# Optimization experiments

Measured on AMD Instinct MI355X. Metric: run time of the kernel, lower is better.

Reference implementation:

```python
import jax, jax.numpy as jnp
import numpy as np

N_NODES = 50000
N_EDGES = 800000
IN_DIM = 128
HID = 64
OUT_DIM = 128
N_GRAPHS = 256


def setup_inputs() -> dict:
    key = jax.random.key(0)
    ks = jax.random.split(key, 8)
    x = jax.random.normal(ks[0], (N_NODES, IN_DIM), dtype=jnp.float32)
    edge_index = jax.random.randint(ks[1], (2, N_EDGES), 0, N_NODES, dtype=jnp.int64)
    batch = jnp.sort(jax.random.randint(ks[2], (N_NODES,), 0, N_GRAPHS, dtype=jnp.int64))
    # Glorot-ish init for GCN weights, zero bias (PyG default bias=True)
    W1 = jax.random.normal(ks[3], (IN_DIM, HID), dtype=jnp.float32) / np.sqrt(IN_DIM)
    b1 = jnp.zeros((HID,), dtype=jnp.float32)
    W2 = jax.random.normal(ks[4], (HID, HID), dtype=jnp.float32) / np.sqrt(HID)
    b2 = jnp.zeros((HID,), dtype=jnp.float32)
    W3 = jax.random.normal(ks[5], (HID, OUT_DIM), dtype=jnp.float32) / np.sqrt(HID)
    b3 = jnp.zeros((OUT_DIM,), dtype=jnp.float32)
    return {"x": x, "edge_index": edge_index, "batch": batch, "num_graphs": N_GRAPHS,
            "W1": W1, "b1": b1, "W2": W2, "b2": b2, "W3": W3, "b3": b3}


def _gcn_norm(edge_index, n_nodes):
    # PyG GCNConv default: add self-loops, symmetric D^{-1/2}(A+I)D^{-1/2} norm.
    loops = jnp.arange(n_nodes, dtype=edge_index.dtype)
    src = jnp.concatenate([edge_index[0], loops])  # [E + N]
    dst = jnp.concatenate([edge_index[1], loops])
    deg = jax.ops.segment_sum(jnp.ones_like(dst, dtype=jnp.float32), dst,
                              num_segments=n_nodes)
    dinv = jnp.where(deg > 0, jax.lax.rsqrt(jnp.maximum(deg, 1.0)), 0.0)
    norm = dinv[src] * dinv[dst]  # [E + N]
    return src, dst, norm


def _gcn_conv(x, W, b, src, dst, norm, n_nodes):
    h = x @ W                                  # [N, F_out] dense GEMM
    msg = h[src] * norm[:, None]               # gather + scale  [E+N, F_out]
    agg = jax.ops.segment_sum(msg, dst, num_segments=n_nodes)
    return agg + b


def reference(x, edge_index, batch, num_graphs, W1, b1, W2, b2, W3, b3):
    n_nodes = x.shape[0]
    src, dst, norm = _gcn_norm(edge_index, n_nodes)
    h = jax.nn.gelu(_gcn_conv(x, W1, b1, src, dst, norm, n_nodes))
    h = jax.nn.gelu(_gcn_conv(h, W2, b2, src, dst, norm, n_nodes))
    h = _gcn_conv(h, W3, b3, src, dst, norm, n_nodes)
    # global_mean_pool over batch segment ids
    sums = jax.ops.segment_sum(h, batch, num_segments=num_graphs)
    counts = jax.ops.segment_sum(jnp.ones((n_nodes,), dtype=h.dtype), batch,
                                 num_segments=num_graphs)
    return sums / jnp.maximum(counts, 1.0)[:, None]
```

## Files before the change

kernel.cpp:

```cpp
#include <hip/hip_runtime.h>
#include <hip/hip_fp16.h>
#include <math.h>

#define N_NODES   50000
#define N_EDGES   800000
#define IN_DIM    128
#define HID       64
#define OUT_DIM   128
#define N_GRAPHS  256
#define MAX_DEG   64
#define PARTS     8
#define PSIZE     (N_NODES / PARTS)
#define EPB       4096
#define AGG_NPB   32
#define GEMM_BLKS 782

typedef _Float16 half8 __attribute__((ext_vector_type(8)));
typedef float floatx4 __attribute__((ext_vector_type(4)));


__global__ __launch_bounds__(256) void k_prep_w(const float* __restrict__ W1, __half* __restrict__ Wt1,
                                                const float* __restrict__ W2, __half* __restrict__ Wt2) {
    int blk = blockIdx.x;
    if (blk < 4) {
        int idx = blk * 256 + threadIdx.x;
        int g = idx >> 6, n = idx & 63;
#pragma unroll
        for (int i = 0; i < 8; i++)
            Wt1[idx * 8 + i] = __float2half(W1[(8 * g + i) * 64 + n]);
    } else {
        int idx = (blk - 4) * 256 + threadIdx.x;
        if (idx < 512) {
            int g = idx >> 6, n = idx & 63;
#pragma unroll
            for (int i = 0; i < 8; i++)
                Wt2[idx * 8 + i] = __float2half(W2[(8 * g + i) * 64 + n]);
        }
    }
}


__global__ __launch_bounds__(256) void k_fused1(const float* __restrict__ A,
                                                const __half* __restrict__ Bp,
                                                __half* __restrict__ C,
                                                const int* __restrict__ src,
                                                const int* __restrict__ dst,
                                                int* __restrict__ deg,
                                                int* __restrict__ col) {
    if (blockIdx.x < GEMM_BLKS) {
        constexpr int K = IN_DIM, S = K / 32;
        int wv   = threadIdx.x >> 6;
        int lane = threadIdx.x & 63;
        int quad = lane >> 4, l15 = lane & 15;
        int row0 = blockIdx.x * 64 + wv * 16;
        if (row0 >= N_NODES) return;

        half8 bf[S][4];
#pragma unroll
        for (int s = 0; s < S; s++)
#pragma unroll
            for (int j = 0; j < 4; j++)
                bf[s][j] = *(const half8*)(Bp + ((size_t)((4 * s + quad) * 64 + 16 * j + l15)) * 8);

        floatx4 acc[4];
#pragma unroll
        for (int j = 0; j < 4; j++) acc[j] = 0.f;

        int arow = row0 + l15;
#pragma unroll
        for (int s = 0; s < S; s++) {
            float4 xa = *(const float4*)(A + (size_t)arow * K + 32 * s + quad * 8);
            float4 xb = *(const float4*)(A + (size_t)arow * K + 32 * s + quad * 8 + 4);
            half8 af;
            af[0] = (_Float16)xa.x; af[1] = (_Float16)xa.y;
            af[2] = (_Float16)xa.z; af[3] = (_Float16)xa.w;
            af[4] = (_Float16)xb.x; af[5] = (_Float16)xb.y;
            af[6] = (_Float16)xb.z; af[7] = (_Float16)xb.w;
#pragma unroll
            for (int j = 0; j < 4; j++)
                acc[j] = __builtin_amdgcn_mfma_f32_16x16x32_f16(af, bf[s][j], acc[j], 0, 0, 0);
        }
#pragma unroll
        for (int j = 0; j < 4; j++)
#pragma unroll
            for (int r = 0; r < 4; r++)
                C[(size_t)(row0 + quad * 4 + r) * 64 + 16 * j + l15] = __float2half(acc[j][r]);
    } else {
        int bid   = blockIdx.x - GEMM_BLKS;
        int p     = bid & (PARTS - 1);
        int chunk = bid >> 3;
        int e0    = chunk * EPB + threadIdx.x * 16;
        if (e0 + 16 > N_EDGES) return;
        int lo = p * PSIZE, hi = lo + PSIZE;

        int dd[16], ss[16];
        const int4* d4 = (const int4*)(dst + e0);
        const int4* s4 = (const int4*)(src + e0);
#pragma unroll
        for (int j = 0; j < 4; j++) {
            int4 q = d4[j];
            dd[4 * j + 0] = q.x; dd[4 * j + 1] = q.y;
            dd[4 * j + 2] = q.z; dd[4 * j + 3] = q.w;
        }
#pragma unroll
        for (int j = 0; j < 4; j++) {
            int4 q = s4[j];
            ss[4 * j + 0] = q.x; ss[4 * j + 1] = q.y;
            ss[4 * j + 2] = q.z; ss[4 * j + 3] = q.w;
        }

        int pos[16];
#pragma unroll
        for (int j = 0; j < 16; j++) {
            pos[j] = -1;
            if (dd[j] >= lo && dd[j] < hi) pos[j] = atomicAdd(&deg[dd[j]], 1);
        }
#pragma unroll
        for (int j = 0; j < 16; j++) {
            if (pos[j] >= 0 && pos[j] < MAX_DEG)
                col[(size_t)dd[j] * MAX_DEG + pos[j]] = ss[j];
        }
    }
}


__global__ __launch_bounds__(256) void k_prep2(const int* __restrict__ deg,
                                               float* __restrict__ dinv) {
    int n = blockIdx.x * 256 + threadIdx.x;
    if (n < N_NODES) dinv[n] = rsqrtf((float)(deg[n] + 1));
}


__global__ __launch_bounds__(256) void k_mfma2(const __half* __restrict__ A,
                                               const __half* __restrict__ Bp,
                                               __half* __restrict__ C) {
    constexpr int K = HID, S = K / 32;
    int wv   = threadIdx.x >> 6;
    int lane = threadIdx.x & 63;
    int quad = lane >> 4, l15 = lane & 15;
    int row0 = blockIdx.x * 64 + wv * 16;
    if (row0 >= N_NODES) return;

    half8 bf[S][4];
#pragma unroll
    for (int s = 0; s < S; s++)
#pragma unroll
        for (int j = 0; j < 4; j++)
            bf[s][j] = *(const half8*)(Bp + ((size_t)((4 * s + quad) * 64 + 16 * j + l15)) * 8);

    floatx4 acc[4];
#pragma unroll
    for (int j = 0; j < 4; j++) acc[j] = 0.f;

    int arow = row0 + l15;
#pragma unroll
    for (int s = 0; s < S; s++) {
        half8 af = *(const half8*)(A + (size_t)arow * K + 32 * s + quad * 8);
#pragma unroll
        for (int j = 0; j < 4; j++)
            acc[j] = __builtin_amdgcn_mfma_f32_16x16x32_f16(af, bf[s][j], acc[j], 0, 0, 0);
    }
#pragma unroll
    for (int j = 0; j < 4; j++)
#pragma unroll
        for (int r = 0; r < 4; r++)
            C[(size_t)(row0 + quad * 4 + r) * 64 + 16 * j + l15] = __float2half(acc[j][r]);
}


__device__ __forceinline__ void fma8(float* acc, uint4 v, float w) {
    const __half2* h = (const __half2*)&v;
#pragma unroll
    for (int j = 0; j < 4; j++) {
        acc[2 * j]     += w * __low2float(h[j]);
        acc[2 * j + 1] += w * __high2float(h[j]);
    }
}

__global__ __launch_bounds__(256) void k_agg(const __half* __restrict__ T,
                                             const int* __restrict__ col,
                                             const int* __restrict__ indeg,
                                             const float* __restrict__ dinv,
                                             const float* __restrict__ b,
                                             __half* __restrict__ OUT,
                                             int mode, int scale_src) {
    __shared__ int cols[AGG_NPB][MAX_DEG + 1];
    __shared__ int sdeg[AGG_NPB];
    int base = blockIdx.x * AGG_NPB;

    if (threadIdx.x < AGG_NPB) {
        int g = base + threadIdx.x;
        int dg0 = (g < N_NODES) ? indeg[g] : 0;
        sdeg[threadIdx.x] = dg0 > MAX_DEG ? MAX_DEG : dg0;
    }
    __syncthreads();

    for (int idx = threadIdx.x; idx < AGG_NPB * MAX_DEG; idx += 256) {
        int r = idx >> 6, j = idx & 63;
        if (j < sdeg[r]) cols[r][j] = col[(size_t)(base + r) * MAX_DEG + j];
    }
    __syncthreads();

    int lane = threadIdx.x & 63;
    int wv   = threadIdx.x >> 6;
    int q = lane >> 3, t = lane & 7;
    int local = wv * 8 + q;
    int d = base + local;
    if (d >= N_NODES) return;

    int dg = sdeg[local];
    float dv = dinv[d];

    float acc[8];
#pragma unroll
    for (int j = 0; j < 8; j++) acc[j] = 0.f;
    fma8(acc, *(const uint4*)(T + (size_t)d * HID + t * 8), scale_src ? dv : 1.0f);

    const int* cl = cols[local];
    int i = 0;
    for (; i + 4 <= dg; i += 4) {
        int s0 = cl[i], s1 = cl[i + 1], s2 = cl[i + 2], s3 = cl[i + 3];
        uint4 v0 = *(const uint4*)(T + (size_t)s0 * HID + t * 8);
        uint4 v1 = *(const uint4*)(T + (size_t)s1 * HID + t * 8);
        uint4 v2 = *(const uint4*)(T + (size_t)s2 * HID + t * 8);
        uint4 v3 = *(const uint4*)(T + (size_t)s3 * HID + t * 8);
        float w0 = 1.f, w1 = 1.f, w2 = 1.f, w3 = 1.f;
        if (scale_src) { w0 = dinv[s0]; w1 = dinv[s1]; w2 = dinv[s2]; w3 = dinv[s3]; }
        fma8(acc, v0, w0); fma8(acc, v1, w1); fma8(acc, v2, w2); fma8(acc, v3, w3);
    }
    for (; i < dg; i++) {
        int s = cl[i];
        float w = scale_src ? dinv[s] : 1.f;
        fma8(acc, *(const uint4*)(T + (size_t)s * HID + t * 8), w);
    }

    float o[8];
#pragma unroll
    for (int j = 0; j < 8; j++) o[j] = acc[j] * dv;
    if (mode == 0) {
#pragma unroll
        for (int j = 0; j < 8; j++) {
            float v = o[j] + b[t * 8 + j];
            float u2 = 0.7978845608028654f * (v + 0.044715f * v * v * v);
            float th = 1.0f - 2.0f / (__expf(2.0f * u2) + 1.0f);
            o[j] = 0.5f * v * (1.0f + th) * dv;
        }
    }
    __half2 hh[4];
#pragma unroll
    for (int j = 0; j < 4; j++) hh[j] = __floats2half2_rn(o[2 * j], o[2 * j + 1]);
    *(uint4*)(OUT + (size_t)d * HID + t * 8) = *(uint4*)hh;
}


__global__ __launch_bounds__(256) void k_pool_out(const __half* __restrict__ A,
                                                  const int* __restrict__ batch,
                                                  const float* __restrict__ W3,
                                                  const float* __restrict__ b3,
                                                  float* __restrict__ out) {
    int g = blockIdx.x;
    int lo = 0, hi = N_NODES;
    while (lo < hi) { int m = (lo + hi) >> 1; if (batch[m] < g) lo = m + 1; else hi = m; }
    int lo2 = lo, hi2 = N_NODES;
    while (lo2 < hi2) { int m = (lo2 + hi2) >> 1; if (batch[m] < g + 1) lo2 = m + 1; else hi2 = m; }
    int start = lo, end = lo2;

    int lane = threadIdx.x & 63;
    int wave = threadIdx.x >> 6;
    float acc = 0.f;
    for (int n = start + wave; n < end; n += 4)
        acc += __half2float(A[(size_t)n * HID + lane]);

    __shared__ float part[4][HID];
    __shared__ float pooled[HID];
    part[wave][lane] = acc;
    __syncthreads();
    if (threadIdx.x < HID)
        pooled[threadIdx.x] = part[0][threadIdx.x] + part[1][threadIdx.x] +
                              part[2][threadIdx.x] + part[3][threadIdx.x];
    __syncthreads();

    if (threadIdx.x < OUT_DIM) {
        float cntf = (float)(end - start);
        float inv = 1.0f / fmaxf(cntf, 1.0f);
        float s = 0.f;
#pragma unroll
        for (int k = 0; k < HID; k++) s += pooled[k] * W3[k * OUT_DIM + threadIdx.x];
        out[g * OUT_DIM + threadIdx.x] = (s + cntf * b3[threadIdx.x]) * inv;
    }
}


extern "C" void kernel_launch(void* const* d_in, const int* in_sizes, int n_in,
                              void* d_out, int out_size, void* d_ws, size_t ws_size,
                              hipStream_t stream) {
    const float* x     = (const float*)d_in[0];
    const int*   ei    = (const int*)d_in[1];
    const int*   batch = (const int*)d_in[2];
    const float* W1    = (const float*)d_in[4];
    const float* b1    = (const float*)d_in[5];
    const float* W2    = (const float*)d_in[6];
    const float* b2    = (const float*)d_in[7];
    const float* W3    = (const float*)d_in[8];
    const float* b3    = (const float*)d_in[9];
    float* out = (float*)d_out;

    const int* esrc = ei;
    const int* edst = ei + N_EDGES;

    int*    deg  = (int*)d_ws;
    float*  dinv = (float*)(deg + N_NODES);
    int*    col  = (int*)(dinv + N_NODES);
    __half* t    = (__half*)(col + (size_t)N_NODES * MAX_DEG);
    __half* p    = t + (size_t)N_NODES * HID;
    __half* Wt1  = p + (size_t)N_NODES * HID;
    __half* Wt2  = Wt1 + IN_DIM * HID;

    (void)hipMemsetAsync(deg, 0, (size_t)N_NODES * 4, stream);

    const int CHUNKS = (N_EDGES + EPB - 1) / EPB;
    const int AB = (N_NODES + AGG_NPB - 1) / AGG_NPB;

    k_prep_w<<<6, 256, 0, stream>>>(W1, Wt1, W2, Wt2);
    k_fused1<<<GEMM_BLKS + CHUNKS * PARTS, 256, 0, stream>>>(x, Wt1, t, esrc, edst, deg, col);
    k_prep2<<<196, 256, 0, stream>>>(deg, dinv);

    k_agg<<<AB, 256, 0, stream>>>(t, col, deg, dinv, b1, p, 0, 1);
    k_mfma2<<<GEMM_BLKS, 256, 0, stream>>>(p, Wt2, t);
    k_agg<<<AB, 256, 0, stream>>>(t, col, deg, dinv, b2, p, 0, 0);
    k_agg<<<AB, 256, 0, stream>>>(p, col, deg, dinv, b3, t, 1, 0);
    k_pool_out<<<N_GRAPHS, 256, 0, stream>>>(t, batch, W3, b3, out);
}
```

Measured before the change: 219.8 us.

## Fuse layer-1 aggregation with layer-2 GEMM and compute dinv inline

Folds the layer-2 MFMA GEMM into the first aggregation kernel: each block stages its aggregated, GELU'd rows in shared memory and multiplies them by W2 before writing. It also drops the dinv precompute kernel and array, recomputing rsqrt(deg+1) on the fly from the degree array. This removes two launches and one round trip of the N x 64 intermediate through global memory. In exchange there is an extra gather of indeg per neighbour in the first layer, plus rsqrt arithmetic.

Result: no change. 222.7 us (+1.3%).

```diff
diff --git a/kernel.cpp b/kernel.cpp
--- a/kernel.cpp
+++ b/kernel.cpp
@@ -124,50 +124,6 @@
 }
 
 
-__global__ __launch_bounds__(256) void k_prep2(const int* __restrict__ deg,
-                                               float* __restrict__ dinv) {
-    int n = blockIdx.x * 256 + threadIdx.x;
-    if (n < N_NODES) dinv[n] = rsqrtf((float)(deg[n] + 1));
-}
-
-
-__global__ __launch_bounds__(256) void k_mfma2(const __half* __restrict__ A,
-                                               const __half* __restrict__ Bp,
-                                               __half* __restrict__ C) {
-    constexpr int K = HID, S = K / 32;
-    int wv   = threadIdx.x >> 6;
-    int lane = threadIdx.x & 63;
-    int quad = lane >> 4, l15 = lane & 15;
-    int row0 = blockIdx.x * 64 + wv * 16;
-    if (row0 >= N_NODES) return;
-
-    half8 bf[S][4];
-#pragma unroll
-    for (int s = 0; s < S; s++)
-#pragma unroll
-        for (int j = 0; j < 4; j++)
-            bf[s][j] = *(const half8*)(Bp + ((size_t)((4 * s + quad) * 64 + 16 * j + l15)) * 8);
-
-    floatx4 acc[4];
-#pragma unroll
-    for (int j = 0; j < 4; j++) acc[j] = 0.f;
-
-    int arow = row0 + l15;
-#pragma unroll
-    for (int s = 0; s < S; s++) {
-        half8 af = *(const half8*)(A + (size_t)arow * K + 32 * s + quad * 8);
-#pragma unroll
-        for (int j = 0; j < 4; j++)
-            acc[j] = __builtin_amdgcn_mfma_f32_16x16x32_f16(af, bf[s][j], acc[j], 0, 0, 0);
-    }
-#pragma unroll
-    for (int j = 0; j < 4; j++)
-#pragma unroll
-        for (int r = 0; r < 4; r++)
-            C[(size_t)(row0 + quad * 4 + r) * 64 + 16 * j + l15] = __float2half(acc[j][r]);
-}
-
-
 __device__ __forceinline__ void fma8(float* acc, uint4 v, float w) {
     const __half2* h = (const __half2*)&v;
 #pragma unroll
@@ -177,13 +133,113 @@
     }
 }
 
+
+__global__ __launch_bounds__(256) void k_agg_mm(const __half* __restrict__ T,
+                                                const int* __restrict__ col,
+                                                const int* __restrict__ indeg,
+                                                const float* __restrict__ b,
+                                                const __half* __restrict__ Bp,
+                                                __half* __restrict__ OUT) {
+    __shared__ int cols[AGG_NPB][MAX_DEG + 1];
+    __shared__ int sdeg[AGG_NPB];
+    __shared__ __half p_tile[AGG_NPB][72];
+    int base = blockIdx.x * AGG_NPB;
+
+    if (threadIdx.x < AGG_NPB) {
+        int g = base + threadIdx.x;
+        int dg0 = (g < N_NODES) ? indeg[g] : 0;
+        sdeg[threadIdx.x] = dg0 > MAX_DEG ? MAX_DEG : dg0;
+    }
+    __syncthreads();
+
+    for (int idx = threadIdx.x; idx < AGG_NPB * MAX_DEG; idx += 256) {
+        int r = idx >> 6, j = idx & 63;
+        if (j < sdeg[r]) cols[r][j] = col[(size_t)(base + r) * MAX_DEG + j];
+    }
+    __syncthreads();
+
+    int lane = threadIdx.x & 63;
+    int wv   = threadIdx.x >> 6;
+    int q = lane >> 3, t = lane & 7;
+    int local = wv * 8 + q;
+    int d = base + local;
+
+    if (d < N_NODES) {
+        int dg = sdeg[local];
+        float dv = rsqrtf((float)(indeg[d] + 1));
+
+        float acc[8];
+#pragma unroll
+        for (int j = 0; j < 8; j++) acc[j] = 0.f;
+        fma8(acc, *(const uint4*)(T + (size_t)d * HID + t * 8), dv);
+
+        const int* cl = cols[local];
+        int i = 0;
+        for (; i + 4 <= dg; i += 4) {
+            int s0 = cl[i], s1 = cl[i + 1], s2 = cl[i + 2], s3 = cl[i + 3];
+            uint4 v0 = *(const uint4*)(T + (size_t)s0 * HID + t * 8);
+            uint4 v1 = *(const uint4*)(T + (size_t)s1 * HID + t * 8);
+            uint4 v2 = *(const uint4*)(T + (size_t)s2 * HID + t * 8);
+            uint4 v3 = *(const uint4*)(T + (size_t)s3 * HID + t * 8);
+            float w0 = rsqrtf((float)(indeg[s0] + 1));
+            float w1 = rsqrtf((float)(indeg[s1] + 1));
+            float w2 = rsqrtf((float)(indeg[s2] + 1));
+            float w3 = rsqrtf((float)(indeg[s3] + 1));
+            fma8(acc, v0, w0); fma8(acc, v1, w1); fma8(acc, v2, w2); fma8(acc, v3, w3);
+        }
+        for (; i < dg; i++) {
+            int s = cl[i];
+            fma8(acc, *(const uint4*)(T + (size_t)s * HID + t * 8), rsqrtf((float)(indeg[s] + 1)));
+        }
+
+        half8 hrow;
+#pragma unroll
+        for (int j = 0; j < 8; j++) {
+            float v = acc[j] * dv + b[t * 8 + j];
+            float u2 = 0.7978845608028654f * (v + 0.044715f * v * v * v);
+            float th = 1.0f - 2.0f / (__expf(2.0f * u2) + 1.0f);
+            hrow[j] = (_Float16)(0.5f * v * (1.0f + th) * dv);
+        }
+        *(half8*)&p_tile[local][t * 8] = hrow;
+    }
+    __syncthreads();
+
+    int quad = lane >> 4, l15 = lane & 15;
+    int rows16 = (wv >> 1) * 16;
+    int j0 = (wv & 1) * 2;
+    if (base + rows16 < N_NODES) {
+        half8 bfr[2][2];
+#pragma unroll
+        for (int s = 0; s < 2; s++)
+#pragma unroll
+            for (int jj = 0; jj < 2; jj++)
+                bfr[s][jj] = *(const half8*)(Bp + ((size_t)((4 * s + quad) * 64 + 16 * (j0 + jj) + l15)) * 8);
+
+        floatx4 acc2[2];
+        acc2[0] = 0.f; acc2[1] = 0.f;
+#pragma unroll
+        for (int s = 0; s < 2; s++) {
+            half8 a = *(const half8*)&p_tile[rows16 + l15][s * 32 + quad * 8];
+            acc2[0] = __builtin_amdgcn_mfma_f32_16x16x32_f16(a, bfr[s][0], acc2[0], 0, 0, 0);
+            acc2[1] = __builtin_amdgcn_mfma_f32_16x16x32_f16(a, bfr[s][1], acc2[1], 0, 0, 0);
+        }
+#pragma unroll
+        for (int jj = 0; jj < 2; jj++)
+#pragma unroll
+            for (int r = 0; r < 4; r++) {
+                int row = base + rows16 + quad * 4 + r;
+                if (row < N_NODES)
+                    OUT[(size_t)row * 64 + 16 * (j0 + jj) + l15] = __float2half(acc2[jj][r]);
+            }
+    }
+}
+
+
 __global__ __launch_bounds__(256) void k_agg(const __half* __restrict__ T,
                                              const int* __restrict__ col,
                                              const int* __restrict__ indeg,
-                                             const float* __restrict__ dinv,
                                              const float* __restrict__ b,
-                                             __half* __restrict__ OUT,
-                                             int mode, int scale_src) {
+                                             __half* __restrict__ OUT, int mode) {
     __shared__ int cols[AGG_NPB][MAX_DEG + 1];
     __shared__ int sdeg[AGG_NPB];
     int base = blockIdx.x * AGG_NPB;
@@ -209,12 +265,12 @@
     if (d >= N_NODES) return;
 
     int dg = sdeg[local];
-    float dv = dinv[d];
+    float dv = rsqrtf((float)(indeg[d] + 1));
 
     float acc[8];
 #pragma unroll
     for (int j = 0; j < 8; j++) acc[j] = 0.f;
-    fma8(acc, *(const uint4*)(T + (size_t)d * HID + t * 8), scale_src ? dv : 1.0f);
+    fma8(acc, *(const uint4*)(T + (size_t)d * HID + t * 8), 1.0f);
 
     const int* cl = cols[local];
     int i = 0;
@@ -224,14 +280,11 @@
         uint4 v1 = *(const uint4*)(T + (size_t)s1 * HID + t * 8);
         uint4 v2 = *(const uint4*)(T + (size_t)s2 * HID + t * 8);
         uint4 v3 = *(const uint4*)(T + (size_t)s3 * HID + t * 8);
-        float w0 = 1.f, w1 = 1.f, w2 = 1.f, w3 = 1.f;
-        if (scale_src) { w0 = dinv[s0]; w1 = dinv[s1]; w2 = dinv[s2]; w3 = dinv[s3]; }
-        fma8(acc, v0, w0); fma8(acc, v1, w1); fma8(acc, v2, w2); fma8(acc, v3, w3);
+        fma8(acc, v0, 1.f); fma8(acc, v1, 1.f); fma8(acc, v2, 1.f); fma8(acc, v3, 1.f);
     }
     for (; i < dg; i++) {
         int s = cl[i];
-        float w = scale_src ? dinv[s] : 1.f;
-        fma8(acc, *(const uint4*)(T + (size_t)s * HID + t * 8), w);
+        fma8(acc, *(const uint4*)(T + (size_t)s * HID + t * 8), 1.f);
     }
 
     float o[8];
@@ -309,8 +362,7 @@
     const int* edst = ei + N_EDGES;
 
     int*    deg  = (int*)d_ws;
-    float*  dinv = (float*)(deg + N_NODES);
-    int*    col  = (int*)(dinv + N_NODES);
+    int*    col  = deg + N_NODES;
     __half* t    = (__half*)(col + (size_t)N_NODES * MAX_DEG);
     __half* p    = t + (size_t)N_NODES * HID;
     __half* Wt1  = p + (size_t)N_NODES * HID;
@@ -323,11 +375,9 @@
 
     k_prep_w<<<6, 256, 0, stream>>>(W1, Wt1, W2, Wt2);
     k_fused1<<<GEMM_BLKS + CHUNKS * PARTS, 256, 0, stream>>>(x, Wt1, t, esrc, edst, deg, col);
-    k_prep2<<<196, 256, 0, stream>>>(deg, dinv);
-
-    k_agg<<<AB, 256, 0, stream>>>(t, col, deg, dinv, b1, p, 0, 1);
-    k_mfma2<<<GEMM_BLKS, 256, 0, stream>>>(p, Wt2, t);
-    k_agg<<<AB, 256, 0, stream>>>(t, col, deg, dinv, b2, p, 0, 0);
-    k_agg<<<AB, 256, 0, stream>>>(p, col, deg, dinv, b3, t, 1, 0);
-    k_pool_out<<<N_GRAPHS, 256, 0, stream>>>(t, batch, W3, b3, out);
-}
+
+    k_agg_mm<<<AB, 256, 0, stream>>>(t, col, deg, b1, Wt2, p);
+    k_agg<<<AB, 256, 0, stream>>>(p, col, deg, b2, t, 0);
+    k_agg<<<AB, 256, 0, stream>>>(t, col, deg, b3, p, 1);
+    k_pool_out<<<N_GRAPHS, 256, 0, stream>>>(p, batch, W3, b3, out);
+}
```

## Split features into two 32-wide planes and fold weight and dinv prep into kernels

Applied to the files above, without the earlier changes.

Node feature buffers are stored as two 32-column half planes. Each aggregation block now handles one plane, with 4 lanes per node instead of 8, so the gathered working set per pass is halved and may stay in cache. The separate weight-transpose and dinv kernels are removed: GEMM blocks convert the weights to half in LDS, and dinv is recomputed with rsqrt from degrees inside aggregation. The LDS staging of column indices is dropped, so neighbour indices are read straight from global memory and every edge pays an extra degree load for the source scaling.

Result: slower. 232.2 us (+5.7%).

```diff
diff --git a/kernel.cpp b/kernel.cpp
--- a/kernel.cpp
+++ b/kernel.cpp
@@ -12,36 +12,16 @@
 #define PARTS     8
 #define PSIZE     (N_NODES / PARTS)
 #define EPB       4096
-#define AGG_NPB   32
+#define AGG_NPB   64
 #define GEMM_BLKS 782
+#define PSTRIDE   ((size_t)N_NODES * 32)
 
 typedef _Float16 half8 __attribute__((ext_vector_type(8)));
 typedef float floatx4 __attribute__((ext_vector_type(4)));
 
 
-__global__ __launch_bounds__(256) void k_prep_w(const float* __restrict__ W1, __half* __restrict__ Wt1,
-                                                const float* __restrict__ W2, __half* __restrict__ Wt2) {
-    int blk = blockIdx.x;
-    if (blk < 4) {
-        int idx = blk * 256 + threadIdx.x;
-        int g = idx >> 6, n = idx & 63;
-#pragma unroll
-        for (int i = 0; i < 8; i++)
-            Wt1[idx * 8 + i] = __float2half(W1[(8 * g + i) * 64 + n]);
-    } else {
-        int idx = (blk - 4) * 256 + threadIdx.x;
-        if (idx < 512) {
-            int g = idx >> 6, n = idx & 63;
-#pragma unroll
-            for (int i = 0; i < 8; i++)
-                Wt2[idx * 8 + i] = __float2half(W2[(8 * g + i) * 64 + n]);
-        }
-    }
-}
-
-
 __global__ __launch_bounds__(256) void k_fused1(const float* __restrict__ A,
-                                                const __half* __restrict__ Bp,
+                                                const float* __restrict__ W1,
                                                 __half* __restrict__ C,
                                                 const int* __restrict__ src,
                                                 const int* __restrict__ dst,
@@ -49,6 +29,21 @@
                                                 int* __restrict__ col) {
     if (blockIdx.x < GEMM_BLKS) {
         constexpr int K = IN_DIM, S = K / 32;
+        __shared__ __half wlds[IN_DIM * HID];
+
+#pragma unroll
+        for (int u = 0; u < 8; u++) {
+            int o = threadIdx.x * 32 + u * 4;
+            float4 w = *(const float4*)(W1 + o);
+            int k = o >> 6, n = o & 63;
+            int bi = (((k >> 3) * 64) + n) * 8 + (k & 7);
+            wlds[bi]      = __float2half(w.x);
+            wlds[bi + 8]  = __float2half(w.y);
+            wlds[bi + 16] = __float2half(w.z);
+            wlds[bi + 24] = __float2half(w.w);
+        }
+        __syncthreads();
+
         int wv   = threadIdx.x >> 6;
         int lane = threadIdx.x & 63;
         int quad = lane >> 4, l15 = lane & 15;
@@ -60,7 +55,7 @@
         for (int s = 0; s < S; s++)
 #pragma unroll
             for (int j = 0; j < 4; j++)
-                bf[s][j] = *(const half8*)(Bp + ((size_t)((4 * s + quad) * 64 + 16 * j + l15)) * 8);
+                bf[s][j] = *(const half8*)&wlds[(((4 * s + quad) * 64) + 16 * j + l15) * 8];
 
         floatx4 acc[4];
 #pragma unroll
@@ -84,7 +79,8 @@
         for (int j = 0; j < 4; j++)
 #pragma unroll
             for (int r = 0; r < 4; r++)
-                C[(size_t)(row0 + quad * 4 + r) * 64 + 16 * j + l15] = __float2half(acc[j][r]);
+                C[(size_t)(j >> 1) * PSTRIDE + (size_t)(row0 + quad * 4 + r) * 32 +
+                  16 * (j & 1) + l15] = __float2half(acc[j][r]);
     } else {
         int bid   = blockIdx.x - GEMM_BLKS;
         int p     = bid & (PARTS - 1);
@@ -124,17 +120,101 @@
 }
 
 
-__global__ __launch_bounds__(256) void k_prep2(const int* __restrict__ deg,
-                                               float* __restrict__ dinv) {
-    int n = blockIdx.x * 256 + threadIdx.x;
-    if (n < N_NODES) dinv[n] = rsqrtf((float)(deg[n] + 1));
+__device__ __forceinline__ void fma8(float* acc, uint4 v, float w) {
+    const __half2* h = (const __half2*)&v;
+#pragma unroll
+    for (int j = 0; j < 4; j++) {
+        acc[2 * j]     += w * __low2float(h[j]);
+        acc[2 * j + 1] += w * __high2float(h[j]);
+    }
+}
+
+
+__global__ __launch_bounds__(256) void k_agg(const __half* __restrict__ T,
+                                             const int* __restrict__ col,
+                                             const int* __restrict__ indeg,
+                                             const float* __restrict__ b,
+                                             __half* __restrict__ OUT,
+                                             int mode, int scale_src) {
+    int plane = blockIdx.x & 1;
+    int base  = (blockIdx.x >> 1) * AGG_NPB;
+    int lane = threadIdx.x & 63;
+    int wv   = threadIdx.x >> 6;
+    int q = lane >> 2, t = lane & 3;
+    int local = wv * 16 + q;
+    int d = base + local;
+    if (d >= N_NODES) return;
+
+    int dgf = indeg[d];
+    int dg = dgf > MAX_DEG ? MAX_DEG : dgf;
+    float dv = rsqrtf((float)(dgf + 1));
+    const __half* P = T + (size_t)plane * PSTRIDE;
+
+    float acc[8];
+#pragma unroll
+    for (int j = 0; j < 8; j++) acc[j] = 0.f;
+    fma8(acc, *(const uint4*)(P + (size_t)d * 32 + t * 8), scale_src ? dv : 1.0f);
+
+    const int* cl = col + (size_t)d * MAX_DEG;
+    int i = 0;
+    for (; i + 4 <= dg; i += 4) {
+        int s0 = cl[i], s1 = cl[i + 1], s2 = cl[i + 2], s3 = cl[i + 3];
+        uint4 v0 = *(const uint4*)(P + (size_t)s0 * 32 + t * 8);
+        uint4 v1 = *(const uint4*)(P + (size_t)s1 * 32 + t * 8);
+        uint4 v2 = *(const uint4*)(P + (size_t)s2 * 32 + t * 8);
+        uint4 v3 = *(const uint4*)(P + (size_t)s3 * 32 + t * 8);
+        float w0 = 1.f, w1 = 1.f, w2 = 1.f, w3 = 1.f;
+        if (scale_src) {
+            w0 = rsqrtf((float)(indeg[s0] + 1));
+            w1 = rsqrtf((float)(indeg[s1] + 1));
+            w2 = rsqrtf((float)(indeg[s2] + 1));
+            w3 = rsqrtf((float)(indeg[s3] + 1));
+        }
+        fma8(acc, v0, w0); fma8(acc, v1, w1); fma8(acc, v2, w2); fma8(acc, v3, w3);
+    }
+    for (; i < dg; i++) {
+        int s = cl[i];
+        float w = scale_src ? rsqrtf((float)(indeg[s] + 1)) : 1.f;
+        fma8(acc, *(const uint4*)(P + (size_t)s * 32 + t * 8), w);
+    }
+
+    float o[8];
+#pragma unroll
+    for (int j = 0; j < 8; j++) o[j] = acc[j] * dv;
+    if (mode == 0) {
+#pragma unroll
+        for (int j = 0; j < 8; j++) {
+            float v = o[j] + b[plane * 32 + t * 8 + j];
+            float u2 = 0.7978845608028654f * (v + 0.044715f * v * v * v);
+            float th = 1.0f - 2.0f / (__expf(2.0f * u2) + 1.0f);
+            o[j] = 0.5f * v * (1.0f + th) * dv;
+        }
+    }
+    __half2 hh[4];
+#pragma unroll
+    for (int j = 0; j < 4; j++) hh[j] = __floats2half2_rn(o[2 * j], o[2 * j + 1]);
+    *(uint4*)(OUT + (size_t)plane * PSTRIDE + (size_t)d * 32 + t * 8) = *(uint4*)hh;
 }
 
 
 __global__ __launch_bounds__(256) void k_mfma2(const __half* __restrict__ A,
-                                               const __half* __restrict__ Bp,
+                                               const float* __restrict__ W2,
                                                __half* __restrict__ C) {
-    constexpr int K = HID, S = K / 32;
+    constexpr int S = HID / 32;
+    __shared__ __half wlds[HID * HID];
+#pragma unroll
+    for (int u = 0; u < 4; u++) {
+        int o = threadIdx.x * 16 + u * 4;
+        float4 w = *(const float4*)(W2 + o);
+        int k = o >> 6, n = o & 63;
+        int bi = (((k >> 3) * 64) + n) * 8 + (k & 7);
+        wlds[bi]      = __float2half(w.x);
+        wlds[bi + 8]  = __float2half(w.y);
+        wlds[bi + 16] = __float2half(w.z);
+        wlds[bi + 24] = __float2half(w.w);
+    }
+    __syncthreads();
+
     int wv   = threadIdx.x >> 6;
     int lane = threadIdx.x & 63;
     int quad = lane >> 4, l15 = lane & 15;
@@ -146,7 +226,7 @@
     for (int s = 0; s < S; s++)
 #pragma unroll
         for (int j = 0; j < 4; j++)
-            bf[s][j] = *(const half8*)(Bp + ((size_t)((4 * s + quad) * 64 + 16 * j + l15)) * 8);
+            bf[s][j] = *(const half8*)&wlds[(((4 * s + quad) * 64) + 16 * j + l15) * 8];
 
     floatx4 acc[4];
 #pragma unroll
@@ -155,7 +235,7 @@
     int arow = row0 + l15;
 #pragma unroll
     for (int s = 0; s < S; s++) {
-        half8 af = *(const half8*)(A + (size_t)arow * K + 32 * s + quad * 8);
+        half8 af = *(const half8*)(A + (size_t)s * PSTRIDE + (size_t)arow * 32 + quad * 8);
 #pragma unroll
         for (int j = 0; j < 4; j++)
             acc[j] = __builtin_amdgcn_mfma_f32_16x16x32_f16(af, bf[s][j], acc[j], 0, 0, 0);
@@ -164,92 +244,8 @@
     for (int j = 0; j < 4; j++)
 #pragma unroll
         for (int r = 0; r < 4; r++)
-            C[(size_t)(row0 + quad * 4 + r) * 64 + 16 * j + l15] = __float2half(acc[j][r]);
-}
-
-
-__device__ __forceinline__ void fma8(float* acc, uint4 v, float w) {
-    const __half2* h = (const __half2*)&v;
-#pragma unroll
-    for (int j = 0; j < 4; j++) {
-        acc[2 * j]     += w * __low2float(h[j]);
-        acc[2 * j + 1] += w * __high2float(h[j]);
-    }
-}
-
-__global__ __launch_bounds__(256) void k_agg(const __half* __restrict__ T,
-                                             const int* __restrict__ col,
-                                             const int* __restrict__ indeg,
-                                             const float* __restrict__ dinv,
-                                             const float* __restrict__ b,
-                                             __half* __restrict__ OUT,
-                                             int mode, int scale_src) {
-    __shared__ int cols[AGG_NPB][MAX_DEG + 1];
-    __shared__ int sdeg[AGG_NPB];
-    int base = blockIdx.x * AGG_NPB;
-
-    if (threadIdx.x < AGG_NPB) {
-        int g = base + threadIdx.x;
-        int dg0 = (g < N_NODES) ? indeg[g] : 0;
-        sdeg[threadIdx.x] = dg0 > MAX_DEG ? MAX_DEG : dg0;
-    }
-    __syncthreads();
-
-    for (int idx = threadIdx.x; idx < AGG_NPB * MAX_DEG; idx += 256) {
-        int r = idx >> 6, j = idx & 63;
-        if (j < sdeg[r]) cols[r][j] = col[(size_t)(base + r) * MAX_DEG + j];
-    }
-    __syncthreads();
-
-    int lane = threadIdx.x & 63;
-    int wv   = threadIdx.x >> 6;
-    int q = lane >> 3, t = lane & 7;
-    int local = wv * 8 + q;
-    int d = base + local;
-    if (d >= N_NODES) return;
-
-    int dg = sdeg[local];
-    float dv = dinv[d];
-
-    float acc[8];
-#pragma unroll
-    for (int j = 0; j < 8; j++) acc[j] = 0.f;
-    fma8(acc, *(const uint4*)(T + (size_t)d * HID + t * 8), scale_src ? dv : 1.0f);
-
-    const int* cl = cols[local];
-    int i = 0;
-    for (; i + 4 <= dg; i += 4) {
-        int s0 = cl[i], s1 = cl[i + 1], s2 = cl[i + 2], s3 = cl[i + 3];
-        uint4 v0 = *(const uint4*)(T + (size_t)s0 * HID + t * 8);
-        uint4 v1 = *(const uint4*)(T + (size_t)s1 * HID + t * 8);
-        uint4 v2 = *(const uint4*)(T + (size_t)s2 * HID + t * 8);
-        uint4 v3 = *(const uint4*)(T + (size_t)s3 * HID + t * 8);
-        float w0 = 1.f, w1 = 1.f, w2 = 1.f, w3 = 1.f;
-        if (scale_src) { w0 = dinv[s0]; w1 = dinv[s1]; w2 = dinv[s2]; w3 = dinv[s3]; }
-        fma8(acc, v0, w0); fma8(acc, v1, w1); fma8(acc, v2, w2); fma8(acc, v3, w3);
-    }
-    for (; i < dg; i++) {
-        int s = cl[i];
-        float w = scale_src ? dinv[s] : 1.f;
-        fma8(acc, *(const uint4*)(T + (size_t)s * HID + t * 8), w);
-    }
-
-    float o[8];
-#pragma unroll
-    for (int j = 0; j < 8; j++) o[j] = acc[j] * dv;
-    if (mode == 0) {
-#pragma unroll
-        for (int j = 0; j < 8; j++) {
-            float v = o[j] + b[t * 8 + j];
-            float u2 = 0.7978845608028654f * (v + 0.044715f * v * v * v);
-            float th = 1.0f - 2.0f / (__expf(2.0f * u2) + 1.0f);
-            o[j] = 0.5f * v * (1.0f + th) * dv;
-        }
-    }
-    __half2 hh[4];
-#pragma unroll
-    for (int j = 0; j < 4; j++) hh[j] = __floats2half2_rn(o[2 * j], o[2 * j + 1]);
-    *(uint4*)(OUT + (size_t)d * HID + t * 8) = *(uint4*)hh;
+            C[(size_t)(j >> 1) * PSTRIDE + (size_t)(row0 + quad * 4 + r) * 32 +
+              16 * (j & 1) + l15] = __float2half(acc[j][r]);
 }
 
 
@@ -267,9 +263,10 @@
 
     int lane = threadIdx.x & 63;
     int wave = threadIdx.x >> 6;
+    const __half* Ap = A + (size_t)(lane >> 5) * PSTRIDE + (lane & 31);
     float acc = 0.f;
     for (int n = start + wave; n < end; n += 4)
-        acc += __half2float(A[(size_t)n * HID + lane]);
+        acc += __half2float(Ap[(size_t)n * 32]);
 
     __shared__ float part[4][HID];
     __shared__ float pooled[HID];
@@ -309,25 +306,19 @@
     const int* edst = ei + N_EDGES;
 
     int*    deg  = (int*)d_ws;
-    float*  dinv = (float*)(deg + N_NODES);
-    int*    col  = (int*)(dinv + N_NODES);
+    int*    col  = deg + N_NODES;
     __half* t    = (__half*)(col + (size_t)N_NODES * MAX_DEG);
-    __half* p    = t + (size_t)N_NODES * HID;
-    __half* Wt1  = p + (size_t)N_NODES * HID;
-    __half* Wt2  = Wt1 + IN_DIM * HID;
+    __half* p    = t + 2 * PSTRIDE;
 
     (void)hipMemsetAsync(deg, 0, (size_t)N_NODES * 4, stream);
 
     const int CHUNKS = (N_EDGES + EPB - 1) / EPB;
-    const int AB = (N_NODES + AGG_NPB - 1) / AGG_NPB;
-
-    k_prep_w<<<6, 256, 0, stream>>>(W1, Wt1, W2, Wt2);
-    k_fused1<<<GEMM_BLKS + CHUNKS * PARTS, 256, 0, stream>>>(x, Wt1, t, esrc, edst, deg, col);
-    k_prep2<<<196, 256, 0, stream>>>(deg, dinv);
-
-    k_agg<<<AB, 256, 0, stream>>>(t, col, deg, dinv, b1, p, 0, 1);
-    k_mfma2<<<GEMM_BLKS, 256, 0, stream>>>(p, Wt2, t);
-    k_agg<<<AB, 256, 0, stream>>>(t, col, deg, dinv, b2, p, 0, 0);
-    k_agg<<<AB, 256, 0, stream>>>(p, col, deg, dinv, b3, t, 1, 0);
+    const int AB = 2 * ((N_NODES + AGG_NPB - 1) / AGG_NPB);
+
+    k_fused1<<<GEMM_BLKS + CHUNKS * PARTS, 256, 0, stream>>>(x, W1, t, esrc, edst, deg, col);
+    k_agg<<<AB, 256, 0, stream>>>(t, col, deg, b1, p, 0, 1);
+    k_mfma2<<<GEMM_BLKS, 256, 0, stream>>>(p, W2, t);
+    k_agg<<<AB, 256, 0, stream>>>(t, col, deg, b2, p, 0, 0);
+    k_agg<<<AB, 256, 0, stream>>>(p, col, deg, b3, t, 1, 0);
     k_pool_out<<<N_GRAPHS, 256, 0, stream>>>(t, batch, W3, b3, out);
 }
```
